# Performance work log

Measured on AMD Instinct MI355X. Metric: run time of the kernel, lower is better.

## Reference

```python
import jax, jax.numpy as jnp
import numpy as np

EPS = 1e-12  # F.normalize default eps

def l2norm(x, axis=1):
    n = jnp.sqrt(jnp.sum(x * x, axis=axis, keepdims=True))
    return x / jnp.maximum(n, EPS)

def setup_inputs() -> dict:
    key = jax.random.key(0)
    ks = jax.random.split(key, 8)
    N, C, H, W = 32, 1024, 28, 28
    D, K, OUT = 128, 64, 1024
    return {
        "x": jax.random.normal(ks[0], (N, C, H, W), dtype=jnp.float32),
        "Wpool": jax.random.normal(ks[1], (D, C), dtype=jnp.float32) * 0.02,
        "bpool": jax.random.normal(ks[2], (D,), dtype=jnp.float32) * 0.02,
        "Wconv": jax.random.normal(ks[3], (K, D), dtype=jnp.float32) * 0.1,
        "bconv": jax.random.normal(ks[4], (K,), dtype=jnp.float32) * 0.02,
        "centroids": jax.random.uniform(ks[5], (K, D), dtype=jnp.float32),
        "Wproj": jax.random.normal(ks[6], (OUT, K * D), dtype=jnp.float32) * 0.02,
        "bproj": jax.random.normal(ks[7], (OUT,), dtype=jnp.float32) * 0.02,
    }

def reference(x, Wpool, bpool, Wconv, bconv, centroids, Wproj, bproj):
    N, C, H, W = x.shape
    K, D = centroids.shape
    S = H * W
    # 1x1 conv channel pool: (N,C,H,W) -> (N,D,H,W)
    x = jnp.einsum('nchw,dc->ndhw', x, Wpool) + bpool[None, :, None, None]
    # descriptor-wise L2 norm over channel dim
    x = l2norm(x, axis=1)
    xf = x.reshape(N, D, S)                      # (N,D,S)
    # 1x1 conv -> soft assignment logits, softmax over clusters
    sa = jnp.einsum('nds,kd->nks', xf, Wconv) + bconv[None, :, None]
    sa = jax.nn.softmax(sa, axis=1)              # (N,K,S)
    # vlad[n,k,d] = sum_s sa[n,k,s]*(xf[n,d,s] - centroids[k,d])
    #            = (sa @ xf^T) - centroids * sum_s sa   (GEMM rewrite, same math)
    vlad = jnp.einsum('nks,nds->nkd', sa, xf) - centroids[None] * jnp.sum(sa, axis=-1)[:, :, None]
    vlad = l2norm(vlad, axis=1)                  # L2Norm over dim=1 (clusters)
    vlad = vlad.reshape(N, K * D)
    vlad = vlad @ Wproj.T + bproj
    return l2norm(vlad, axis=1)
```

## Files before the change

kernel.cpp:

```cpp
#include <hip/hip_runtime.h>
#include <math.h>

#define NB 32
#define CC 1024
#define SS 784
#define SP 832
#define DD 128
#define KK 64
#define OUTD 1024
#define KD 8192
#define NSPLIT 13
#define PSPLIT 32

#define OFF_XN    0
#define OFF_SA    (OFF_XN + NB*DD*SP*2)
#define OFF_WPK   (OFF_SA + NB*KK*SP*2)
#define OFF_WCK   (OFF_WPK + 32*8*64*8*2)
#define OFF_VLADP (OFF_WCK + 16*64*8*2)
#define OFF_SASUM (OFF_VLADP + NB*NSPLIT*KD*4)
#define OFF_VLADN (OFF_SASUM + NB*NSPLIT*KK*4)
#define OFF_OUTP  (OFF_VLADN + NB*KD*4)

typedef __attribute__((ext_vector_type(8))) short bf16x8;
typedef __attribute__((ext_vector_type(4))) float f32x4;

__device__ __forceinline__ unsigned int pk_bf16(float a, float b) {
    unsigned int ua = __builtin_bit_cast(unsigned int, a);
    unsigned int ub = __builtin_bit_cast(unsigned int, b);
    ua += 0x7FFFu + ((ua >> 16) & 1u);
    ub += 0x7FFFu + ((ub >> 16) & 1u);
    return (ua >> 16) | (ub & 0xFFFF0000u);
}
__device__ __forceinline__ unsigned short f2bf(float a) {
    unsigned int ua = __builtin_bit_cast(unsigned int, a);
    ua += 0x7FFFu + ((ua >> 16) & 1u);
    return (unsigned short)(ua >> 16);
}
__device__ __forceinline__ float bf2f(unsigned short u) {
    unsigned int v = ((unsigned int)u) << 16;
    return __builtin_bit_cast(float, v);
}

__global__ __launch_bounds__(256)
void pack_weights(const float* __restrict__ Wpool, const float* __restrict__ Wconv,
                  unsigned short* __restrict__ Wpk, unsigned short* __restrict__ Wck,
                  unsigned short* __restrict__ sa)
{
    const int b = blockIdx.x;
    const int t = threadIdx.x;
    if (b < 8) {
#pragma unroll
        for (int i = 0; i < 8; i++) {
            const int id = t + 256 * i;
            const int ktl = id >> 9;
            const int mt  = (id >> 6) & 7;
            const int l   = id & 63;
            const int lm = l & 15, quad = l >> 4;
            const int kt = b * 4 + ktl;
            const int d = mt * 16 + lm;
            const int c = kt * 32 + quad * 8;
            const float4 v0 = *(const float4*)&Wpool[(size_t)d * CC + c];
            const float4 v1 = *(const float4*)&Wpool[(size_t)d * CC + c + 4];
            unsigned int* dst = (unsigned int*)&Wpk[(size_t)((kt * 8 + mt) * 64 + l) * 8];
            dst[0] = pk_bf16(v0.x, v0.y); dst[1] = pk_bf16(v0.z, v0.w);
            dst[2] = pk_bf16(v1.x, v1.y); dst[3] = pk_bf16(v1.z, v1.w);
        }
    } else if (b == 8) {
#pragma unroll
        for (int i = 0; i < 4; i++) {
            const int id = t + 256 * i;
            const int tile = id >> 6;
            const int l = id & 63;
            const int lm = l & 15, quad = l >> 4;
            const int k = (tile >> 2) * 16 + lm;
            const int d = (tile & 3) * 32 + quad * 8;
            const float4 v0 = *(const float4*)&Wconv[(size_t)k * DD + d];
            const float4 v1 = *(const float4*)&Wconv[(size_t)k * DD + d + 4];
            unsigned int* dst = (unsigned int*)&Wck[(size_t)(tile * 64 + l) * 8];
            dst[0] = pk_bf16(v0.x, v0.y); dst[1] = pk_bf16(v0.z, v0.w);
            dst[2] = pk_bf16(v1.x, v1.y); dst[3] = pk_bf16(v1.z, v1.w);
        }
    } else {
        const int id  = (b - 9) * 256 + t;
        const int sgrp = id % 12;
        const int rem  = id / 12;
        const int k    = rem & 63;
        const int n    = rem >> 6;
        unsigned long long* p =
            (unsigned long long*)&sa[((size_t)(n * KK + k)) * SP + SS + sgrp * 4];
        *p = 0ull;
    }
}

__global__ __launch_bounds__(256, 4)
void pool_norm_assign(const float* __restrict__ x, const unsigned short* __restrict__ Wpk,
                      const float* __restrict__ bpool, const unsigned short* __restrict__ Wck,
                      const float* __restrict__ bconv,
                      unsigned short* __restrict__ xn, unsigned short* __restrict__ sa)
{
    const int n  = blockIdx.y;
    const int s0 = blockIdx.x * 16;
    const int t  = threadIdx.x;
    const int l  = t & 63;
    const int w  = t >> 6;
    const int lm = l & 15;
    const int quad = l >> 4;

    __shared__ alignas(16) unsigned short Bst[128 * 16 * 8];
    __shared__ alignas(16) unsigned short xnT[16 * 16 * 8];
    __shared__ float red[4][16];
    __shared__ float sums[4][16];

    {
        const int cl = l;
        const int sq = w;
        const float* xb = x + (size_t)n * CC * SS + s0 + sq * 4;
#pragma unroll
        for (int h = 0; h < 2; h++) {
            float4 gv[8];
#pragma unroll
            for (int it = 0; it < 8; it++) {
                const int c = (h * 8 + it) * 64 + cl;
                gv[it] = *(const float4*)(xb + (size_t)c * SS);
            }
#pragma unroll
            for (int it = 0; it < 8; it++) {
                const int c = (h * 8 + it) * 64 + cl;
                const int oct = c >> 3, c7 = c & 7;
                const float* gf = (const float*)&gv[it];
#pragma unroll
                for (int j = 0; j < 4; j++) {
                    const int s = sq * 4 + j;
                    Bst[(size_t)(oct * 16 + (s ^ (oct & 15))) * 8 + c7] = f2bf(gf[j]);
                }
            }
        }
    }
    __syncthreads();

    f32x4 acc[2];
    acc[0] = (f32x4){0.f, 0.f, 0.f, 0.f};
    acc[1] = (f32x4){0.f, 0.f, 0.f, 0.f};

    bf16x8 a_nxt[2];
#pragma unroll
    for (int i = 0; i < 2; i++)
        a_nxt[i] = *(const bf16x8*)&Wpk[(size_t)((w * 2 + i) * 64 + l) * 8];

    for (int kt = 0; kt < 32; kt++) {
        const bf16x8 a0 = a_nxt[0], a1 = a_nxt[1];
        if (kt < 31) {
#pragma unroll
            for (int i = 0; i < 2; i++)
                a_nxt[i] = *(const bf16x8*)&Wpk[(size_t)(((kt + 1) * 8 + w * 2 + i) * 64 + l) * 8];
        }
        const int oct = kt * 4 + quad;
        const bf16x8 bfrag = *(const bf16x8*)&Bst[(size_t)(oct * 16 + (lm ^ (oct & 15))) * 8];
        acc[0] = __builtin_amdgcn_mfma_f32_16x16x32_bf16(a0, bfrag, acc[0], 0, 0, 0);
        acc[1] = __builtin_amdgcn_mfma_f32_16x16x32_bf16(a1, bfrag, acc[1], 0, 0, 0);
    }

    float vals[2][4];
    float ssq = 0.f;
#pragma unroll
    for (int i = 0; i < 2; i++)
#pragma unroll
        for (int r = 0; r < 4; r++) {
            const int d = (w * 2 + i) * 16 + quad * 4 + r;
            const float v = acc[i][r] + bpool[d];
            vals[i][r] = v; ssq += v * v;
        }
    ssq += __shfl_xor(ssq, 16, 64);
    ssq += __shfl_xor(ssq, 32, 64);
    if (quad == 0) red[w][lm] = ssq;
    __syncthreads();
    const float scale = 1.f / fmaxf(sqrtf(red[0][lm] + red[1][lm] + red[2][lm] + red[3][lm]), 1e-12f);
    const int sg = s0 + lm;
    unsigned short* xnp = xn + (size_t)n * DD * SP;
#pragma unroll
    for (int i = 0; i < 2; i++)
#pragma unroll
        for (int r = 0; r < 4; r++) {
            const int d = (w * 2 + i) * 16 + quad * 4 + r;
            const float v = vals[i][r] * scale;
            xnp[(size_t)d * SP + sg] = f2bf(v);
            xnT[(size_t)(((d >> 3) * 16) + lm) * 8 + (d & 7)] = f2bf(v);
        }
    __syncthreads();

    f32x4 acc2 = (f32x4){0.f, 0.f, 0.f, 0.f};
#pragma unroll
    for (int dsv = 0; dsv < 4; dsv++) {
        const bf16x8 bfrag = *(const bf16x8*)&xnT[(size_t)((dsv * 4 + quad) * 16 + lm) * 8];
        const bf16x8 afrag = *(const bf16x8*)&Wck[(size_t)((w * 4 + dsv) * 64 + l) * 8];
        acc2 = __builtin_amdgcn_mfma_f32_16x16x32_bf16(afrag, bfrag, acc2, 0, 0, 0);
    }
    float e[4]; float ps = 0.f;
#pragma unroll
    for (int r = 0; r < 4; r++) {
        const int k = w * 16 + quad * 4 + r;
        e[r] = expf(acc2[r] + bconv[k]);
        ps += e[r];
    }
    ps += __shfl_xor(ps, 16, 64);
    ps += __shfl_xor(ps, 32, 64);
    if (quad == 0) sums[w][lm] = ps;
    __syncthreads();
    const float inv = 1.f / (sums[0][lm] + sums[1][lm] + sums[2][lm] + sums[3][lm]);
    unsigned short* sap = sa + (size_t)n * KK * SP;
#pragma unroll
    for (int r = 0; r < 4; r++) {
        const int k = w * 16 + quad * 4 + r;
        sap[(size_t)k * SP + sg] = f2bf(e[r] * inv);
    }
}

__global__ __launch_bounds__(256)
void vlad_mfma(const unsigned short* __restrict__ xn, const unsigned short* __restrict__ sa,
               float* __restrict__ vladp, float* __restrict__ sasump)
{
    const int p = blockIdx.x;
    const int n = blockIdx.y;
    const int t = threadIdx.x;
    const int l = t & 63;
    const int w = t >> 6;
    const int kth = w & 1, nh = w >> 1;
    const int lm = l & 15, quad = l >> 4;

    const unsigned short* sap = sa + (size_t)n * KK * SP;
    const unsigned short* xnp = xn + (size_t)n * DD * SP;

    f32x4 acc[2][4];
#pragma unroll
    for (int j = 0; j < 2; j++)
#pragma unroll
        for (int i = 0; i < 4; i++) acc[j][i] = (f32x4){0.f, 0.f, 0.f, 0.f};
    float ksum[2] = {0.f, 0.f};

#pragma unroll
    for (int st = 0; st < 2; st++) {
        const int sb = p * 64 + st * 32 + quad * 8;
        bf16x8 af[2], bfv[4];
#pragma unroll
        for (int j = 0; j < 2; j++)
            af[j] = *(const bf16x8*)&sap[(size_t)((kth * 2 + j) * 16 + lm) * SP + sb];
#pragma unroll
        for (int i = 0; i < 4; i++)
            bfv[i] = *(const bf16x8*)&xnp[(size_t)((nh * 4 + i) * 16 + lm) * SP + sb];
#pragma unroll
        for (int j = 0; j < 2; j++)
#pragma unroll
            for (int i = 0; i < 4; i++)
                acc[j][i] = __builtin_amdgcn_mfma_f32_16x16x32_bf16(af[j], bfv[i], acc[j][i], 0, 0, 0);
#pragma unroll
        for (int j = 0; j < 2; j++)
#pragma unroll
            for (int e = 0; e < 8; e++)
                ksum[j] += bf2f((unsigned short)af[j][e]);
    }

    float* vp = vladp + ((size_t)n * NSPLIT + p) * KD;
#pragma unroll
    for (int j = 0; j < 2; j++)
#pragma unroll
        for (int i = 0; i < 4; i++) {
            const int kq = (kth * 2 + j) * 4 + quad;
            const int d  = (nh * 4 + i) * 16 + lm;
            *(f32x4*)&vp[(size_t)(kq * DD + d) * 4] = acc[j][i];
        }

#pragma unroll
    for (int j = 0; j < 2; j++) {
        ksum[j] += __shfl_xor(ksum[j], 16, 64);
        ksum[j] += __shfl_xor(ksum[j], 32, 64);
    }
    if (nh == 0 && quad == 0) {
#pragma unroll
        for (int j = 0; j < 2; j++)
            sasump[((size_t)n * NSPLIT + p) * KK + (kth * 2 + j) * 16 + lm] = ksum[j];
    }
}

__global__ __launch_bounds__(256)
void vlad_finish(const float* __restrict__ vladp, const float* __restrict__ sasump,
                 const float* __restrict__ centroids, float* __restrict__ vladn)
{
    const int dg = blockIdx.x;
    const int n  = blockIdx.y;
    const int t  = threadIdx.x;
    const int kq = t & 15;
    const int d  = dg * 16 + (t >> 4);

    __shared__ float sas[KK];
    if (t < KK) {
        float sm = 0.f;
#pragma unroll
        for (int p = 0; p < NSPLIT; p++) sm += sasump[((size_t)n * NSPLIT + p) * KK + t];
        sas[t] = sm;
    }
    __syncthreads();

    f32x4 v = (f32x4){0.f, 0.f, 0.f, 0.f};
#pragma unroll
    for (int p = 0; p < NSPLIT; p++) {
        const f32x4 pr = *(const f32x4*)&vladp[((size_t)n * NSPLIT + p) * KD + (size_t)(kq * DD + d) * 4];
        v += pr;
    }
#pragma unroll
    for (int r = 0; r < 4; r++)
        v[r] -= centroids[(size_t)(kq * 4 + r) * DD + d] * sas[kq * 4 + r];

    float ssq = v[0] * v[0] + v[1] * v[1] + v[2] * v[2] + v[3] * v[3];
    ssq += __shfl_xor(ssq, 1, 64);
    ssq += __shfl_xor(ssq, 2, 64);
    ssq += __shfl_xor(ssq, 4, 64);
    ssq += __shfl_xor(ssq, 8, 64);
    const float scale = 1.f / fmaxf(sqrtf(ssq), 1e-12f);

    float* vo = vladn + (size_t)n * KD;
#pragma unroll
    for (int r = 0; r < 4; r++)
        vo[(size_t)(kq * 4 + r) * DD + d] = v[r] * scale;
}

__global__ __launch_bounds__(256)
void proj_mfma(const float* __restrict__ vladn, const float* __restrict__ Wproj,
               float* __restrict__ outp)
{
    const int o0 = blockIdx.x * 64;
    const int c0 = blockIdx.y * (KD / PSPLIT);
    const int t  = threadIdx.x;
    const int l  = t & 63;
    const int w  = t >> 6;
    const int lm = l & 15, quad = l >> 4;
    const int o  = o0 + w * 16 + lm;

    f32x4 acc[2];
    acc[0] = (f32x4){0.f, 0.f, 0.f, 0.f};
    acc[1] = (f32x4){0.f, 0.f, 0.f, 0.f};

#pragma unroll 2
    for (int kt = 0; kt < 8; kt++) {
        const int c = c0 + kt * 32 + quad * 8;
        const float4 b0 = *(const float4*)&Wproj[(size_t)o * KD + c];
        const float4 b1 = *(const float4*)&Wproj[(size_t)o * KD + c + 4];
        float4 a00 = *(const float4*)&vladn[(size_t)(0 * 16 + lm) * KD + c];
        float4 a01 = *(const float4*)&vladn[(size_t)(0 * 16 + lm) * KD + c + 4];
        float4 a10 = *(const float4*)&vladn[(size_t)(16 + lm) * KD + c];
        float4 a11 = *(const float4*)&vladn[(size_t)(16 + lm) * KD + c + 4];
        union { unsigned int u[4]; bf16x8 v; } ub, ua0, ua1;
        ub.u[0] = pk_bf16(b0.x, b0.y); ub.u[1] = pk_bf16(b0.z, b0.w);
        ub.u[2] = pk_bf16(b1.x, b1.y); ub.u[3] = pk_bf16(b1.z, b1.w);
        ua0.u[0] = pk_bf16(a00.x, a00.y); ua0.u[1] = pk_bf16(a00.z, a00.w);
        ua0.u[2] = pk_bf16(a01.x, a01.y); ua0.u[3] = pk_bf16(a01.z, a01.w);
        ua1.u[0] = pk_bf16(a10.x, a10.y); ua1.u[1] = pk_bf16(a10.z, a10.w);
        ua1.u[2] = pk_bf16(a11.x, a11.y); ua1.u[3] = pk_bf16(a11.z, a11.w);
        acc[0] = __builtin_amdgcn_mfma_f32_16x16x32_bf16(ua0.v, ub.v, acc[0], 0, 0, 0);
        acc[1] = __builtin_amdgcn_mfma_f32_16x16x32_bf16(ua1.v, ub.v, acc[1], 0, 0, 0);
    }

#pragma unroll
    for (int a = 0; a < 2; a++)
#pragma unroll
        for (int r = 0; r < 4; r++) {
            const int nn = a * 16 + quad * 4 + r;
            outp[((size_t)blockIdx.y * NB + nn) * OUTD + o] = acc[a][r];
        }
}

__global__ __launch_bounds__(256)
void final_norm_kernel(const float* __restrict__ outp, const float* __restrict__ bproj,
                       float* __restrict__ out)
{
    const int n = blockIdx.x;
    const int t = threadIdx.x;
    const int o4 = t * 4;

    float4 a = *(const float4*)&bproj[o4];
#pragma unroll
    for (int p = 0; p < PSPLIT; p++) {
        const float4 pr = *(const float4*)&outp[((size_t)p * NB + n) * OUTD + o4];
        a.x += pr.x; a.y += pr.y; a.z += pr.z; a.w += pr.w;
    }
    float ssp = a.x * a.x + a.y * a.y + a.z * a.z + a.w * a.w;
#pragma unroll
    for (int off = 32; off > 0; off >>= 1) ssp += __shfl_down(ssp, off, 64);
    __shared__ float rs[4];
    if ((t & 63) == 0) rs[t >> 6] = ssp;
    __syncthreads();
    const float total = rs[0] + rs[1] + rs[2] + rs[3];
    const float scale = 1.f / fmaxf(sqrtf(total), 1e-12f);
    float4 o;
    o.x = a.x * scale; o.y = a.y * scale; o.z = a.z * scale; o.w = a.w * scale;
    *(float4*)&out[(size_t)n * OUTD + o4] = o;
}

extern "C" void kernel_launch(void* const* d_in, const int* in_sizes, int n_in,
                              void* d_out, int out_size, void* d_ws, size_t ws_size,
                              hipStream_t stream)
{
    const float* x         = (const float*)d_in[0];
    const float* Wpool     = (const float*)d_in[1];
    const float* bpool     = (const float*)d_in[2];
    const float* Wconv     = (const float*)d_in[3];
    const float* bconv     = (const float*)d_in[4];
    const float* centroids = (const float*)d_in[5];
    const float* Wproj     = (const float*)d_in[6];
    const float* bproj     = (const float*)d_in[7];
    float* out = (float*)d_out;
    char*  wsb = (char*)d_ws;

    unsigned short* xn     = (unsigned short*)(wsb + OFF_XN);
    unsigned short* sa     = (unsigned short*)(wsb + OFF_SA);
    unsigned short* Wpk    = (unsigned short*)(wsb + OFF_WPK);
    unsigned short* Wck    = (unsigned short*)(wsb + OFF_WCK);
    float*          vladp  = (float*)(wsb + OFF_VLADP);
    float*          sasump = (float*)(wsb + OFF_SASUM);
    float*          vladn  = (float*)(wsb + OFF_VLADN);
    float*          outp   = (float*)(wsb + OFF_OUTP);

    pack_weights<<<dim3(105), 256, 0, stream>>>(Wpool, Wconv, Wpk, Wck, sa);
    pool_norm_assign<<<dim3(SS / 16, NB), 256, 0, stream>>>(x, Wpk, bpool, Wck, bconv, xn, sa);
    vlad_mfma<<<dim3(NSPLIT, NB), 256, 0, stream>>>(xn, sa, vladp, sasump);
    vlad_finish<<<dim3(DD / 16, NB), 256, 0, stream>>>(vladp, sasump, centroids, vladn);
    proj_mfma<<<dim3(OUTD / 64, PSPLIT), 256, 0, stream>>>(vladn, Wproj, outp);
    final_norm_kernel<<<dim3(NB), 256, 0, stream>>>(outp, bproj, out);
}
```

Baseline: 241.8 us.

## Rework x load pattern, split VLAD GEMM over D, widen final norm

```diff
diff --git a/kernel.cpp b/kernel.cpp
--- a/kernel.cpp
+++ b/kernel.cpp
@@ -112,28 +112,33 @@
     __shared__ float sums[4][16];
 
     {
-        const int cl = l;
-        const int sq = w;
-        const float* xb = x + (size_t)n * CC * SS + s0 + sq * 4;
-#pragma unroll
-        for (int h = 0; h < 2; h++) {
-            float4 gv[8];
-#pragma unroll
-            for (int it = 0; it < 8; it++) {
-                const int c = (h * 8 + it) * 64 + cl;
-                gv[it] = *(const float4*)(xb + (size_t)c * SS);
-            }
-#pragma unroll
-            for (int it = 0; it < 8; it++) {
-                const int c = (h * 8 + it) * 64 + cl;
-                const int oct = c >> 3, c7 = c & 7;
-                const float* gf = (const float*)&gv[it];
-#pragma unroll
-                for (int j = 0; j < 4; j++) {
-                    const int s = sq * 4 + j;
-                    Bst[(size_t)(oct * 16 + (s ^ (oct & 15))) * 8 + c7] = f2bf(gf[j]);
-                }
-            }
+        const int s_h = l & 7;
+        const int cr  = l >> 3;
+        const int sl0 = 2 * s_h;
+        const float* xb = x + (size_t)n * CC * SS + s0 + sl0;
+        const int cw = w * 256 + cr;
+
+        float2 ga[16], gb[16];
+#pragma unroll
+        for (int it = 0; it < 16; it++)
+            ga[it] = *(const float2*)(xb + (size_t)(cw + it * 8) * SS);
+#pragma unroll
+        for (int it = 0; it < 16; it++)
+            gb[it] = *(const float2*)(xb + (size_t)(cw + 128 + it * 8) * SS);
+
+#pragma unroll
+        for (int it = 0; it < 16; it++) {
+            const int oct = w * 32 + it;
+            const int sw = it & 15;
+            Bst[(size_t)(oct * 16 + (sl0 ^ sw)) * 8 + cr]       = f2bf(ga[it].x);
+            Bst[(size_t)(oct * 16 + ((sl0 + 1) ^ sw)) * 8 + cr] = f2bf(ga[it].y);
+        }
+#pragma unroll
+        for (int it = 0; it < 16; it++) {
+            const int oct = w * 32 + 16 + it;
+            const int sw = it & 15;
+            Bst[(size_t)(oct * 16 + (sl0 ^ sw)) * 8 + cr]       = f2bf(gb[it].x);
+            Bst[(size_t)(oct * 16 + ((sl0 + 1) ^ sw)) * 8 + cr] = f2bf(gb[it].y);
         }
     }
     __syncthreads();
@@ -221,63 +226,50 @@
 {
     const int p = blockIdx.x;
     const int n = blockIdx.y;
+    const int z = blockIdx.z;
     const int t = threadIdx.x;
     const int l = t & 63;
     const int w = t >> 6;
-    const int kth = w & 1, nh = w >> 1;
     const int lm = l & 15, quad = l >> 4;
 
     const unsigned short* sap = sa + (size_t)n * KK * SP;
     const unsigned short* xnp = xn + (size_t)n * DD * SP;
 
-    f32x4 acc[2][4];
-#pragma unroll
-    for (int j = 0; j < 2; j++)
-#pragma unroll
-        for (int i = 0; i < 4; i++) acc[j][i] = (f32x4){0.f, 0.f, 0.f, 0.f};
-    float ksum[2] = {0.f, 0.f};
+    f32x4 acc[4];
+#pragma unroll
+    for (int i = 0; i < 4; i++) acc[i] = (f32x4){0.f, 0.f, 0.f, 0.f};
+    float ksum = 0.f;
 
 #pragma unroll
     for (int st = 0; st < 2; st++) {
         const int sb = p * 64 + st * 32 + quad * 8;
-        bf16x8 af[2], bfv[4];
-#pragma unroll
-        for (int j = 0; j < 2; j++)
-            af[j] = *(const bf16x8*)&sap[(size_t)((kth * 2 + j) * 16 + lm) * SP + sb];
+        const bf16x8 af = *(const bf16x8*)&sap[(size_t)(w * 16 + lm) * SP + sb];
+        bf16x8 bfv[4];
 #pragma unroll
         for (int i = 0; i < 4; i++)
-            bfv[i] = *(const bf16x8*)&xnp[(size_t)((nh * 4 + i) * 16 + lm) * SP + sb];
-#pragma unroll
-        for (int j = 0; j < 2; j++)
-#pragma unroll
-            for (int i = 0; i < 4; i++)
-                acc[j][i] = __builtin_amdgcn_mfma_f32_16x16x32_bf16(af[j], bfv[i], acc[j][i], 0, 0, 0);
-#pragma unroll
-        for (int j = 0; j < 2; j++)
-#pragma unroll
-            for (int e = 0; e < 8; e++)
-                ksum[j] += bf2f((unsigned short)af[j][e]);
+            bfv[i] = *(const bf16x8*)&xnp[(size_t)((z * 4 + i) * 16 + lm) * SP + sb];
+#pragma unroll
+        for (int i = 0; i < 4; i++)
+            acc[i] = __builtin_amdgcn_mfma_f32_16x16x32_bf16(af, bfv[i], acc[i], 0, 0, 0);
+        if (z == 0) {
+#pragma unroll
+            for (int e = 0; e < 8; e++) ksum += bf2f((unsigned short)af[e]);
+        }
     }
 
     float* vp = vladp + ((size_t)n * NSPLIT + p) * KD;
-#pragma unroll
-    for (int j = 0; j < 2; j++)
-#pragma unroll
-        for (int i = 0; i < 4; i++) {
-            const int kq = (kth * 2 + j) * 4 + quad;
-            const int d  = (nh * 4 + i) * 16 + lm;
-            *(f32x4*)&vp[(size_t)(kq * DD + d) * 4] = acc[j][i];
-        }
-
-#pragma unroll
-    for (int j = 0; j < 2; j++) {
-        ksum[j] += __shfl_xor(ksum[j], 16, 64);
-        ksum[j] += __shfl_xor(ksum[j], 32, 64);
-    }
-    if (nh == 0 && quad == 0) {
-#pragma unroll
-        for (int j = 0; j < 2; j++)
-            sasump[((size_t)n * NSPLIT + p) * KK + (kth * 2 + j) * 16 + lm] = ksum[j];
+    const int kq = w * 4 + quad;
+#pragma unroll
+    for (int i = 0; i < 4; i++) {
+        const int d = (z * 4 + i) * 16 + lm;
+        *(f32x4*)&vp[(size_t)(kq * DD + d) * 4] = acc[i];
+    }
+
+    if (z == 0) {
+        ksum += __shfl_xor(ksum, 16, 64);
+        ksum += __shfl_xor(ksum, 32, 64);
+        if (quad == 0)
+            sasump[((size_t)n * NSPLIT + p) * KK + w * 16 + lm] = ksum;
     }
 }
 
@@ -339,7 +331,7 @@
     acc[0] = (f32x4){0.f, 0.f, 0.f, 0.f};
     acc[1] = (f32x4){0.f, 0.f, 0.f, 0.f};
 
-#pragma unroll 2
+#pragma unroll 4
     for (int kt = 0; kt < 8; kt++) {
         const int c = c0 + kt * 32 + quad * 8;
         const float4 b0 = *(const float4*)&Wproj[(size_t)o * KD + c];
@@ -368,31 +360,29 @@
         }
 }
 
-__global__ __launch_bounds__(256)
+__global__ __launch_bounds__(1024)
 void final_norm_kernel(const float* __restrict__ outp, const float* __restrict__ bproj,
                        float* __restrict__ out)
 {
     const int n = blockIdx.x;
     const int t = threadIdx.x;
-    const int o4 = t * 4;
-
-    float4 a = *(const float4*)&bproj[o4];
-#pragma unroll
-    for (int p = 0; p < PSPLIT; p++) {
-        const float4 pr = *(const float4*)&outp[((size_t)p * NB + n) * OUTD + o4];
-        a.x += pr.x; a.y += pr.y; a.z += pr.z; a.w += pr.w;
-    }
-    float ssp = a.x * a.x + a.y * a.y + a.z * a.z + a.w * a.w;
+
+    float a = bproj[t];
+#pragma unroll
+    for (int p = 0; p < PSPLIT; p++)
+        a += outp[((size_t)p * NB + n) * OUTD + t];
+
+    float ssp = a * a;
 #pragma unroll
     for (int off = 32; off > 0; off >>= 1) ssp += __shfl_down(ssp, off, 64);
-    __shared__ float rs[4];
+    __shared__ float rs[16];
     if ((t & 63) == 0) rs[t >> 6] = ssp;
     __syncthreads();
-    const float total = rs[0] + rs[1] + rs[2] + rs[3];
+    float total = 0.f;
+#pragma unroll
+    for (int g = 0; g < 16; g++) total += rs[g];
     const float scale = 1.f / fmaxf(sqrtf(total), 1e-12f);
-    float4 o;
-    o.x = a.x * scale; o.y = a.y * scale; o.z = a.z * scale; o.w = a.w * scale;
-    *(float4*)&out[(size_t)n * OUTD + o4] = o;
+    out[(size_t)n * OUTD + t] = a * scale;
 }
 
 extern "C" void kernel_launch(void* const* d_in, const int* in_sizes, int n_in,
@@ -421,8 +411,8 @@
 
     pack_weights<<<dim3(105), 256, 0, stream>>>(Wpool, Wconv, Wpk, Wck, sa);
     pool_norm_assign<<<dim3(SS / 16, NB), 256, 0, stream>>>(x, Wpk, bpool, Wck, bconv, xn, sa);
-    vlad_mfma<<<dim3(NSPLIT, NB), 256, 0, stream>>>(xn, sa, vladp, sasump);
+    vlad_mfma<<<dim3(NSPLIT, NB, 2), 256, 0, stream>>>(xn, sa, vladp, sasump);
     vlad_finish<<<dim3(DD / 16, NB), 256, 0, stream>>>(vladp, sasump, centroids, vladn);
     proj_mfma<<<dim3(OUTD / 64, PSPLIT), 256, 0, stream>>>(vladn, Wproj, outp);
-    final_norm_kernel<<<dim3(NB), 256, 0, stream>>>(outp, bproj, out);
-}
+    final_norm_kernel<<<dim3(NB), 1024, 0, stream>>>(outp, bproj, out);
+}
```

Result: no change. 237.8 us (-1.6%).
